# Kernel optimization log

Hardware: AMD Instinct MI355X
Metric: run time of the kernel (lower is better)

## Reference

```python
import jax, jax.numpy as jnp
import numpy as np
import math

L, N, D = 1024, 64, 64
O = 1024

def setup_inputs() -> dict:
    key = jax.random.key(0)
    k1, k2 = jax.random.split(key)
    x = jax.random.normal(k1, (L, N, D), dtype=jnp.float32)
    upfold = jax.random.normal(k2, (O, N, D), dtype=jnp.float32)
    return {"x": x, "upfold": upfold}

def reference(x, upfold):
    # x: [L, N, D], upfold: [O, N, D]
    d = x.shape[-1]
    scale = 1.0 / math.sqrt(d)
    # affinities: [L, O, N]
    affinities = jnp.einsum('lnd,ond->lon', x, upfold) * scale
    # weighted sum with (sigmoid - 0.5) weights: [L, N, D]
    features = jnp.einsum('lon,ond->lnd', jax.nn.sigmoid(affinities) - 0.5, upfold)
    return features
```

## Files before the change

kernel.cpp:

```cpp
#include <hip/hip_runtime.h>
#include <stdint.h>

#define L_DIM 1024
#define N_DIM 64
#define D_DIM 64
#define O_DIM 1024
#define ND    4096
#define NT    8

typedef float    floatx16 __attribute__((ext_vector_type(16)));
typedef _Float16 half8    __attribute__((ext_vector_type(8)));
typedef _Float16 h2       __attribute__((ext_vector_type(2)));
typedef __fp16   fp16x2   __attribute__((ext_vector_type(2)));

#define IMG_BYTES 16384
#define WS_NEEDED ((size_t)N_DIM * 16 * IMG_BYTES)

#define BUF_STRIDE_FB 17920

__device__ __forceinline__ uint32_t pkh2(float a, float b) {
    fp16x2 p = __builtin_amdgcn_cvt_pkrtz(a, b);
    return __builtin_bit_cast(uint32_t, p);
}

__device__ __forceinline__ half8 mk_frag(uint32_t a, uint32_t b, uint32_t c, uint32_t d) {
    union { uint32_t u[4]; half8 v; } U;
    U.u[0] = a; U.u[1] = b; U.u[2] = c; U.u[3] = d;
    return U.v;
}

__device__ __forceinline__ uint32_t psig(float s0, float s1) {
    const h2 HI = {(_Float16)41.6f,        (_Float16)41.6f};
    const h2 LO = {(_Float16)-41.6f,       (_Float16)-41.6f};
    const h2 SC = {(_Float16)0.0625f,      (_Float16)0.0625f};
    const h2 C0 = {(_Float16)0.03099238f,  (_Float16)0.03099238f};
    const h2 C1 = {(_Float16)-0.00842090f, (_Float16)-0.00842090f};
    const h2 C2 = {(_Float16)0.00151845f,  (_Float16)0.00151845f};
    const h2 C3 = {(_Float16)-1.02197e-4f, (_Float16)-1.02197e-4f};
    h2 s = __builtin_bit_cast(h2, pkh2(s0, s1));
    s = __builtin_elementwise_min(s, HI);
    s = __builtin_elementwise_max(s, LO);
    h2 ha = s * SC;
    h2 v  = ha * ha;
    h2 w  = C2 + v * C3;
    w     = C1 + v * w;
    w     = C0 + v * w;
    h2 f  = s * w;
    return __builtin_bit_cast(uint32_t, f);
}

__device__ __forceinline__ void load_tile(const float* ubase, int ot,
                                          int r8, int c, float4* va, float4* vb) {
    const float* pr = ubase + (size_t)(ot * 64 + 2 * r8) * ND + 4 * c;
    #pragma unroll
    for (int j = 0; j < 2; ++j) {
        va[j] = *(const float4*)(pr + (size_t)(32 * j) * ND);
        vb[j] = *(const float4*)(pr + (size_t)(32 * j) * ND + ND);
    }
}

__global__ void __launch_bounds__(256)
conv_kernel(const float* __restrict__ up, unsigned char* __restrict__ img)
{
    const int tid = threadIdx.x;
    const int r8  = tid >> 4;
    const int c   = tid & 15;
    const int n   = blockIdx.x;
    const int ot  = blockIdx.y;

    const float* ubase = up + (size_t)n * D_DIM;
    float4 va[2], vb[2];
    load_tile(ubase, ot, r8, c, va, vb);

    unsigned char* tb = img + (size_t)(n * 16 + ot) * IMG_BYTES;

    const int kk = c >> 2;
    const int hh = (c >> 1) & 1;
    const int co = (c & 1) * 8;
    #pragma unroll
    for (int j = 0; j < 2; ++j) {
        const int o0 = 2 * r8 + 32 * j;
        unsigned char* g1 = tb + j * 4096 + kk * 1024 + co;
        *(uint2*)(g1 + ((o0 & 31) + 32 * hh) * 16) =
            make_uint2(pkh2(va[j].x, va[j].y), pkh2(va[j].z, va[j].w));
        *(uint2*)(g1 + (((o0 + 1) & 31) + 32 * hh) * 16) =
            make_uint2(pkh2(vb[j].x, vb[j].y), pkh2(vb[j].z, vb[j].w));
    }

    #pragma unroll
    for (int j = 0; j < 2; ++j) {
        const int op   = r8 + 16 * j;
        const int g    = op >> 2;
        const int slot = op & 3;
        const int t2   = g >> 2;
        const int c22  = (g >> 1) & 1;
        const int h2i  = g & 1;
        const float* pa = (const float*)&va[j];
        const float* pb = (const float*)&vb[j];
        #pragma unroll
        for (int col = 0; col < 4; ++col) {
            const int d   = 4 * c + col;
            const int r   = d >> 5;
            const int lane = (d & 31) + 32 * h2i;
            *(uint32_t*)(tb + 8192 + t2 * 4096 + c22 * 2048 + r * 1024
                         + lane * 16 + slot * 4) = pkh2(pa[col], pb[col]);
        }
    }
}

__global__ void __launch_bounds__(512, 4)
corr_kernel_c(const float* __restrict__ x, const unsigned char* __restrict__ img,
              float* __restrict__ out)
{
    __shared__ __align__(16) float Xs[128][68];

    const int tid  = threadIdx.x;
    const int lane = tid & 63;
    const int wid  = tid >> 6;
    const int team = wid >> 2;
    const int tw   = wid & 3;
    const int l31  = lane & 31;
    const int h    = lane >> 5;
    const int n    = blockIdx.x;
    const int lb   = blockIdx.y;
    const int lw   = lb * 128 + tw * 32 + l31;

    const unsigned char* gimg = img + (size_t)n * 16 * IMG_BYTES;

    half8 Xf[4];
    {
        const int xr = tid >> 2;
        const int xq = tid & 3;
        const float* xsrc = x + (size_t)(lb * 128 + xr) * ND + n * D_DIM;
        #pragma unroll
        for (int j = 0; j < 4; ++j) {
            const int f4i = xq * 4 + j;
            *(float4*)&Xs[xr][4 * f4i] = *(const float4*)(xsrc + 4 * f4i);
        }
        __syncthreads();
        const int rl = tw * 32 + l31;
        #pragma unroll
        for (int kk = 0; kk < 4; ++kk) {
            float4 f1 = *(const float4*)&Xs[rl][16 * kk + 8 * h];
            float4 f2 = *(const float4*)&Xs[rl][16 * kk + 8 * h + 4];
            Xf[kk] = mk_frag(pkh2(f1.x, f1.y), pkh2(f1.z, f1.w),
                             pkh2(f2.x, f2.y), pkh2(f2.z, f2.w));
        }
        __syncthreads();
    }

    floatx16 F0, F1;
    #pragma unroll
    for (int i = 0; i < 16; ++i) { F0[i] = 0.0f; F1[i] = 0.0f; }

    for (int ot = 0; ot < 16; ++ot) {
        const unsigned char* tb = gimg + (size_t)ot * IMG_BYTES;

        const unsigned char* g1 = tb + team * 4096 + lane * 16;
        half8 Ak[4];
        #pragma unroll
        for (int kk = 0; kk < 4; ++kk)
            Ak[kk] = *(const half8*)(g1 + kk * 1024);

        floatx16 S;
        #pragma unroll
        for (int i2 = 0; i2 < 16; ++i2) S[i2] = 0.0f;
        #pragma unroll
        for (int kk = 0; kk < 4; ++kk)
            S = __builtin_amdgcn_mfma_f32_32x32x16_f16(Ak[kk], Xf[kk], S, 0, 0, 0);

        uint32_t P[8];
        #pragma unroll
        for (int m = 0; m < 8; ++m) P[m] = psig(S[2*m], S[2*m+1]);

        uint32_t R[4];
        #pragma unroll
        for (int c2 = 0; c2 < 2; ++c2) {
            const int t4 = c2 * 4;
            R[2*c2]   = __shfl_xor(h ? P[t4]     : P[t4 + 2], 32);
            R[2*c2+1] = __shfl_xor(h ? P[t4 + 1] : P[t4 + 3], 32);
        }
        const unsigned char* g2 = tb + 8192 + team * 4096 + lane * 16;
        #pragma unroll
        for (int c2 = 0; c2 < 2; ++c2) {
            const int t4 = c2 * 4;
            half8 B = h ? mk_frag(R[2*c2], R[2*c2+1], P[t4 + 2], P[t4 + 3])
                        : mk_frag(P[t4], P[t4 + 1], R[2*c2], R[2*c2+1]);
            half8 A0 = *(const half8*)(g2 + c2 * 2048);
            half8 A1 = *(const half8*)(g2 + c2 * 2048 + 1024);
            F0 = __builtin_amdgcn_mfma_f32_32x32x16_f16(A0, B, F0, 0, 0, 0);
            F1 = __builtin_amdgcn_mfma_f32_32x32x16_f16(A1, B, F1, 0, 0, 0);
        }
    }

    {
        const int row = tw * 32 + l31;
        if (team == 1) {
            #pragma unroll
            for (int q = 0; q < 4; ++q) {
                float4 a; a.x = F0[4*q]; a.y = F0[4*q+1]; a.z = F0[4*q+2]; a.w = F0[4*q+3];
                *(float4*)&Xs[row][8*q + 4*h] = a;
                float4 bq; bq.x = F1[4*q]; bq.y = F1[4*q+1]; bq.z = F1[4*q+2]; bq.w = F1[4*q+3];
                *(float4*)&Xs[row][32 + 8*q + 4*h] = bq;
            }
        }
        __syncthreads();
        if (team == 0) {
            float* op = out + (size_t)lw * ND + n * D_DIM;
            #pragma unroll
            for (int q = 0; q < 4; ++q) {
                float4 t0 = *(const float4*)&Xs[row][8*q + 4*h];
                float4 a; a.x = F0[4*q]   + t0.x; a.y = F0[4*q+1] + t0.y;
                          a.z = F0[4*q+2] + t0.z; a.w = F0[4*q+3] + t0.w;
                *(float4*)(op + 8*q + 4*h) = a;
                float4 t1 = *(const float4*)&Xs[row][32 + 8*q + 4*h];
                float4 bq; bq.x = F1[4*q]   + t1.x; bq.y = F1[4*q+1] + t1.y;
                           bq.z = F1[4*q+2] + t1.z; bq.w = F1[4*q+3] + t1.w;
                *(float4*)(op + 32 + 8*q + 4*h) = bq;
            }
        }
    }
}

__global__ void __launch_bounds__(512, 4)
corr_kernel_fb(const float* __restrict__ x, const float* __restrict__ up,
               float* __restrict__ out)
{
    __shared__ __align__(16) unsigned char smem[4 * BUF_STRIDE_FB];

    const int tid  = threadIdx.x;
    const int lane = tid & 63;
    const int wid  = tid >> 6;
    const int team = wid >> 2;
    const int tw   = wid & 3;
    const int l31  = lane & 31;
    const int h    = lane >> 5;
    const int ttid = tid & 255;
    const int r8   = ttid >> 4;
    const int c    = ttid & 15;
    const int n    = blockIdx.x;
    const int lb   = blockIdx.y;
    const int lw   = lb * 128 + tw * 32 + l31;

    const float* ubase = up + (size_t)n * D_DIM;
    const int ob = team * NT;
    unsigned char* tsmem = smem + team * 2 * BUF_STRIDE_FB;

    float4 va[2], vb[2];
    load_tile(ubase, ob + 0, r8, c, va, vb);

    half8 Xf[4];
    {
        float (*Xs)[68] = (float (*)[68])smem;
        const int xr = tid >> 2;
        const int xq = tid & 3;
        const float* xsrc = x + (size_t)(lb * 128 + xr) * ND + n * D_DIM;
        #pragma unroll
        for (int j = 0; j < 4; ++j) {
            const int f4i = xq * 4 + j;
            *(float4*)&Xs[xr][4 * f4i] = *(const float4*)(xsrc + 4 * f4i);
        }
        __syncthreads();
        const int rl = tw * 32 + l31;
        #pragma unroll
        for (int kk = 0; kk < 4; ++kk) {
            float4 f1 = *(const float4*)&Xs[rl][16 * kk + 8 * h];
            float4 f2 = *(const float4*)&Xs[rl][16 * kk + 8 * h + 4];
            Xf[kk] = mk_frag(pkh2(f1.x, f1.y), pkh2(f1.z, f1.w),
                             pkh2(f2.x, f2.y), pkh2(f2.z, f2.w));
        }
        __syncthreads();
    }

    #pragma unroll
    for (int j = 0; j < 2; ++j) {
        uint16_t (*Ub)[72]  = (uint16_t (*)[72])(tsmem);
        uint32_t (*Ut2)[68] = (uint32_t (*)[68])(tsmem + 9216);
        *(uint2*)&Ub[2*r8 + 32*j][4*c] =
            make_uint2(pkh2(va[j].x, va[j].y), pkh2(va[j].z, va[j].w));
        *(uint2*)&Ub[2*r8 + 32*j + 1][4*c] =
            make_uint2(pkh2(vb[j].x, vb[j].y), pkh2(vb[j].z, vb[j].w));
        *(uint4*)&Ut2[r8 + 16*j][4*c] =
            make_uint4(pkh2(va[j].x, vb[j].x), pkh2(va[j].y, vb[j].y),
                       pkh2(va[j].z, vb[j].z), pkh2(va[j].w, vb[j].w));
    }
    load_tile(ubase, ob + 1, r8, c, va, vb);
    __syncthreads();

    floatx16 F0, F1;
    #pragma unroll
    for (int i = 0; i < 16; ++i) { F0[i] = 0.0f; F1[i] = 0.0f; }

    for (int ot = 0; ot < NT; ++ot) {
        const int b = ot & 1;
        uint16_t (*Ub)[72]   = (uint16_t (*)[72])(tsmem + b * BUF_STRIDE_FB);
        const uint32_t* utp  = (const uint32_t*)(tsmem + b * BUF_STRIDE_FB + 9216);
        uint16_t (*Ubn)[72]  = (uint16_t (*)[72])(tsmem + (b ^ 1) * BUF_STRIDE_FB);
        uint32_t (*Ut2n)[68] = (uint32_t (*)[68])(tsmem + (b ^ 1) * BUF_STRIDE_FB + 9216);

        half8 A0k[4], A1k[4];
        #pragma unroll
        for (int kk = 0; kk < 4; ++kk) {
            A0k[kk] = *(const half8*)&Ub[l31][16 * kk + 8 * h];
            A1k[kk] = *(const half8*)&Ub[32 + l31][16 * kk + 8 * h];
        }

        if (ot + 1 < NT) {
            #pragma unroll
            for (int j = 0; j < 2; ++j) {
                *(uint2*)&Ubn[2*r8 + 32*j][4*c] =
                    make_uint2(pkh2(va[j].x, va[j].y), pkh2(va[j].z, va[j].w));
                *(uint2*)&Ubn[2*r8 + 32*j + 1][4*c] =
                    make_uint2(pkh2(vb[j].x, vb[j].y), pkh2(vb[j].z, vb[j].w));
                *(uint4*)&Ut2n[r8 + 16*j][4*c] =
                    make_uint4(pkh2(va[j].x, vb[j].x), pkh2(va[j].y, vb[j].y),
                               pkh2(va[j].z, vb[j].z), pkh2(va[j].w, vb[j].w));
            }
        }
        if (ot + 2 < NT)
            load_tile(ubase, ob + ot + 2, r8, c, va, vb);

        floatx16 S0, S1;
        #pragma unroll
        for (int i = 0; i < 16; ++i) { S0[i] = 0.0f; S1[i] = 0.0f; }
        #pragma unroll
        for (int kk = 0; kk < 4; ++kk) {
            S0 = __builtin_amdgcn_mfma_f32_32x32x16_f16(A0k[kk], Xf[kk], S0, 0, 0, 0);
            S1 = __builtin_amdgcn_mfma_f32_32x32x16_f16(A1k[kk], Xf[kk], S1, 0, 0, 0);
        }

        uint32_t P[16];
        #pragma unroll
        for (int m = 0; m < 8; ++m) P[m]     = psig(S0[2*m], S0[2*m+1]);
        #pragma unroll
        for (int m = 0; m < 8; ++m) P[8 + m] = psig(S1[2*m], S1[2*m+1]);

        uint32_t R[8];
        #pragma unroll
        for (int c2 = 0; c2 < 4; ++c2) {
            const uint32_t* Q = P + (c2 >> 1) * 8;
            const int t4 = (c2 & 1) * 4;
            R[2*c2]   = __shfl_xor(h ? Q[t4]     : Q[t4 + 2], 32);
            R[2*c2+1] = __shfl_xor(h ? Q[t4 + 1] : Q[t4 + 3], 32);
        }
        #pragma unroll
        for (int c2 = 0; c2 < 4; ++c2) {
            const uint32_t* Q = P + (c2 >> 1) * 8;
            const int t4 = (c2 & 1) * 4;
            half8 B = h ? mk_frag(R[2*c2], R[2*c2+1], Q[t4 + 2], Q[t4 + 3])
                        : mk_frag(Q[t4], Q[t4 + 1], R[2*c2], R[2*c2+1]);
            const int opb = 8 * c2 + 4 * h;
            uint32_t a0[4], a1[4];
            #pragma unroll
            for (int k = 0; k < 4; ++k) {
                a0[k] = utp[(opb + k) * 68 + l31];
                a1[k] = utp[(opb + k) * 68 + 32 + l31];
            }
            half8 A0 = mk_frag(a0[0], a0[1], a0[2], a0[3]);
            half8 A1 = mk_frag(a1[0], a1[1], a1[2], a1[3]);
            F0 = __builtin_amdgcn_mfma_f32_32x32x16_f16(A0, B, F0, 0, 0, 0);
            F1 = __builtin_amdgcn_mfma_f32_32x32x16_f16(A1, B, F1, 0, 0, 0);
        }
        __syncthreads();
    }

    {
        float (*Fs)[68] = (float (*)[68])smem;
        const int row = tw * 32 + l31;
        if (team == 1) {
            #pragma unroll
            for (int q = 0; q < 4; ++q) {
                float4 a; a.x = F0[4*q]; a.y = F0[4*q+1]; a.z = F0[4*q+2]; a.w = F0[4*q+3];
                *(float4*)&Fs[row][8*q + 4*h] = a;
                float4 bq; bq.x = F1[4*q]; bq.y = F1[4*q+1]; bq.z = F1[4*q+2]; bq.w = F1[4*q+3];
                *(float4*)&Fs[row][32 + 8*q + 4*h] = bq;
            }
        }
        __syncthreads();
        if (team == 0) {
            float* op = out + (size_t)lw * ND + n * D_DIM;
            #pragma unroll
            for (int q = 0; q < 4; ++q) {
                float4 t0 = *(const float4*)&Fs[row][8*q + 4*h];
                float4 a; a.x = F0[4*q]   + t0.x; a.y = F0[4*q+1] + t0.y;
                          a.z = F0[4*q+2] + t0.z; a.w = F0[4*q+3] + t0.w;
                *(float4*)(op + 8*q + 4*h) = a;
                float4 t1 = *(const float4*)&Fs[row][32 + 8*q + 4*h];
                float4 bq; bq.x = F1[4*q]   + t1.x; bq.y = F1[4*q+1] + t1.y;
                           bq.z = F1[4*q+2] + t1.z; bq.w = F1[4*q+3] + t1.w;
                *(float4*)(op + 32 + 8*q + 4*h) = bq;
            }
        }
    }
}

extern "C" void kernel_launch(void* const* d_in, const int* in_sizes, int n_in,
                              void* d_out, int out_size, void* d_ws, size_t ws_size,
                              hipStream_t stream)
{
    const float* x  = (const float*)d_in[0];
    const float* up = (const float*)d_in[1];
    float* out      = (float*)d_out;

    if (d_ws != nullptr && ws_size >= WS_NEEDED) {
        unsigned char* img = (unsigned char*)d_ws;
        conv_kernel<<<dim3(N_DIM, 16), dim3(256), 0, stream>>>(up, img);
        corr_kernel_c<<<dim3(N_DIM, L_DIM / 128), dim3(512), 0, stream>>>(x, img, out);
    } else {
        corr_kernel_fb<<<dim3(N_DIM, L_DIM / 128), dim3(512), 0, stream>>>(x, up, out);
    }
}
```

Baseline: 111.6 us.

## Widen corr kernel to 256 rows per block with double-buffered fragment loads

```diff
diff --git a/kernel.cpp b/kernel.cpp
--- a/kernel.cpp
+++ b/kernel.cpp
@@ -99,8 +99,8 @@
         const float* pb = (const float*)&vb[j];
         #pragma unroll
         for (int col = 0; col < 4; ++col) {
-            const int d   = 4 * c + col;
-            const int r   = d >> 5;
+            const int d    = 4 * c + col;
+            const int r    = d >> 5;
             const int lane = (d & 31) + 32 * h2i;
             *(uint32_t*)(tb + 8192 + t2 * 4096 + c22 * 2048 + r * 1024
                          + lane * 16 + slot * 4) = pkh2(pa[col], pb[col]);
@@ -108,11 +108,65 @@
     }
 }
 
-__global__ void __launch_bounds__(512, 4)
-corr_kernel_c(const float* __restrict__ x, const unsigned char* __restrict__ img,
+__device__ __forceinline__ void load_frags(const unsigned char* tb, int team, int lane,
+                                           half8* Ak, half8* G2) {
+    const unsigned char* g1 = tb + team * 4096 + (size_t)lane * 16;
+    #pragma unroll
+    for (int kk = 0; kk < 4; ++kk)
+        Ak[kk] = *(const half8*)(g1 + kk * 1024);
+    const unsigned char* g2 = tb + 8192 + team * 4096 + (size_t)lane * 16;
+    #pragma unroll
+    for (int i = 0; i < 4; ++i)
+        G2[i] = *(const half8*)(g2 + i * 1024);
+}
+
+__device__ __forceinline__ void compute_tile(const half8* Ak, const half8* G2,
+                                             const half8* Xf0, const half8* Xf1, int h,
+                                             floatx16& F00, floatx16& F01,
+                                             floatx16& F10, floatx16& F11)
+{
+    floatx16 S0, S1;
+    #pragma unroll
+    for (int i = 0; i < 16; ++i) { S0[i] = 0.0f; S1[i] = 0.0f; }
+    #pragma unroll
+    for (int kk = 0; kk < 4; ++kk) {
+        S0 = __builtin_amdgcn_mfma_f32_32x32x16_f16(Ak[kk], Xf0[kk], S0, 0, 0, 0);
+        S1 = __builtin_amdgcn_mfma_f32_32x32x16_f16(Ak[kk], Xf1[kk], S1, 0, 0, 0);
+    }
+
+    uint32_t P0[8], P1[8];
+    #pragma unroll
+    for (int m = 0; m < 8; ++m) { P0[m] = psig(S0[2*m], S0[2*m+1]);
+                                  P1[m] = psig(S1[2*m], S1[2*m+1]); }
+
+    uint32_t R0[4], R1[4];
+    #pragma unroll
+    for (int c2 = 0; c2 < 2; ++c2) {
+        const int t4 = c2 * 4;
+        R0[2*c2]   = __shfl_xor(h ? P0[t4]     : P0[t4 + 2], 32);
+        R0[2*c2+1] = __shfl_xor(h ? P0[t4 + 1] : P0[t4 + 3], 32);
+        R1[2*c2]   = __shfl_xor(h ? P1[t4]     : P1[t4 + 2], 32);
+        R1[2*c2+1] = __shfl_xor(h ? P1[t4 + 1] : P1[t4 + 3], 32);
+    }
+    #pragma unroll
+    for (int c2 = 0; c2 < 2; ++c2) {
+        const int t4 = c2 * 4;
+        half8 B0 = h ? mk_frag(R0[2*c2], R0[2*c2+1], P0[t4 + 2], P0[t4 + 3])
+                     : mk_frag(P0[t4], P0[t4 + 1], R0[2*c2], R0[2*c2+1]);
+        half8 B1 = h ? mk_frag(R1[2*c2], R1[2*c2+1], P1[t4 + 2], P1[t4 + 3])
+                     : mk_frag(P1[t4], P1[t4 + 1], R1[2*c2], R1[2*c2+1]);
+        F00 = __builtin_amdgcn_mfma_f32_32x32x16_f16(G2[2*c2],     B0, F00, 0, 0, 0);
+        F01 = __builtin_amdgcn_mfma_f32_32x32x16_f16(G2[2*c2 + 1], B0, F01, 0, 0, 0);
+        F10 = __builtin_amdgcn_mfma_f32_32x32x16_f16(G2[2*c2],     B1, F10, 0, 0, 0);
+        F11 = __builtin_amdgcn_mfma_f32_32x32x16_f16(G2[2*c2 + 1], B1, F11, 0, 0, 0);
+    }
+}
+
+__global__ void __launch_bounds__(512, 2)
+corr_kernel_w(const float* __restrict__ x, const unsigned char* __restrict__ img,
               float* __restrict__ out)
 {
-    __shared__ __align__(16) float Xs[128][68];
+    __shared__ __align__(16) float Xs[256][68];
 
     const int tid  = threadIdx.x;
     const int lane = tid & 63;
@@ -123,100 +177,86 @@
     const int h    = lane >> 5;
     const int n    = blockIdx.x;
     const int lb   = blockIdx.y;
-    const int lw   = lb * 128 + tw * 32 + l31;
 
     const unsigned char* gimg = img + (size_t)n * 16 * IMG_BYTES;
 
-    half8 Xf[4];
+    half8 Xf0[4], Xf1[4];
     {
-        const int xr = tid >> 2;
-        const int xq = tid & 3;
-        const float* xsrc = x + (size_t)(lb * 128 + xr) * ND + n * D_DIM;
-        #pragma unroll
-        for (int j = 0; j < 4; ++j) {
-            const int f4i = xq * 4 + j;
+        const int xr = tid >> 1;
+        const int xh = tid & 1;
+        const float* xsrc = x + (size_t)(lb * 256 + xr) * ND + n * D_DIM;
+        #pragma unroll
+        for (int j = 0; j < 8; ++j) {
+            const int f4i = xh * 8 + j;
             *(float4*)&Xs[xr][4 * f4i] = *(const float4*)(xsrc + 4 * f4i);
         }
         __syncthreads();
-        const int rl = tw * 32 + l31;
+        const int rl0 = tw * 64 + l31;
+        const int rl1 = rl0 + 32;
         #pragma unroll
         for (int kk = 0; kk < 4; ++kk) {
-            float4 f1 = *(const float4*)&Xs[rl][16 * kk + 8 * h];
-            float4 f2 = *(const float4*)&Xs[rl][16 * kk + 8 * h + 4];
-            Xf[kk] = mk_frag(pkh2(f1.x, f1.y), pkh2(f1.z, f1.w),
-                             pkh2(f2.x, f2.y), pkh2(f2.z, f2.w));
-        }
-        __syncthreads();
-    }
-
-    floatx16 F0, F1;
-    #pragma unroll
-    for (int i = 0; i < 16; ++i) { F0[i] = 0.0f; F1[i] = 0.0f; }
-
-    for (int ot = 0; ot < 16; ++ot) {
-        const unsigned char* tb = gimg + (size_t)ot * IMG_BYTES;
-
-        const unsigned char* g1 = tb + team * 4096 + lane * 16;
-        half8 Ak[4];
-        #pragma unroll
-        for (int kk = 0; kk < 4; ++kk)
-            Ak[kk] = *(const half8*)(g1 + kk * 1024);
-
-        floatx16 S;
-        #pragma unroll
-        for (int i2 = 0; i2 < 16; ++i2) S[i2] = 0.0f;
-        #pragma unroll
-        for (int kk = 0; kk < 4; ++kk)
-            S = __builtin_amdgcn_mfma_f32_32x32x16_f16(Ak[kk], Xf[kk], S, 0, 0, 0);
-
-        uint32_t P[8];
-        #pragma unroll
-        for (int m = 0; m < 8; ++m) P[m] = psig(S[2*m], S[2*m+1]);
-
-        uint32_t R[4];
-        #pragma unroll
-        for (int c2 = 0; c2 < 2; ++c2) {
-            const int t4 = c2 * 4;
-            R[2*c2]   = __shfl_xor(h ? P[t4]     : P[t4 + 2], 32);
-            R[2*c2+1] = __shfl_xor(h ? P[t4 + 1] : P[t4 + 3], 32);
-        }
-        const unsigned char* g2 = tb + 8192 + team * 4096 + lane * 16;
-        #pragma unroll
-        for (int c2 = 0; c2 < 2; ++c2) {
-            const int t4 = c2 * 4;
-            half8 B = h ? mk_frag(R[2*c2], R[2*c2+1], P[t4 + 2], P[t4 + 3])
-                        : mk_frag(P[t4], P[t4 + 1], R[2*c2], R[2*c2+1]);
-            half8 A0 = *(const half8*)(g2 + c2 * 2048);
-            half8 A1 = *(const half8*)(g2 + c2 * 2048 + 1024);
-            F0 = __builtin_amdgcn_mfma_f32_32x32x16_f16(A0, B, F0, 0, 0, 0);
-            F1 = __builtin_amdgcn_mfma_f32_32x32x16_f16(A1, B, F1, 0, 0, 0);
-        }
+            float4 f1 = *(const float4*)&Xs[rl0][16 * kk + 8 * h];
+            float4 f2 = *(const float4*)&Xs[rl0][16 * kk + 8 * h + 4];
+            Xf0[kk] = mk_frag(pkh2(f1.x, f1.y), pkh2(f1.z, f1.w),
+                              pkh2(f2.x, f2.y), pkh2(f2.z, f2.w));
+            float4 f3 = *(const float4*)&Xs[rl1][16 * kk + 8 * h];
+            float4 f4v = *(const float4*)&Xs[rl1][16 * kk + 8 * h + 4];
+            Xf1[kk] = mk_frag(pkh2(f3.x, f3.y), pkh2(f3.z, f3.w),
+                              pkh2(f4v.x, f4v.y), pkh2(f4v.z, f4v.w));
+        }
+        __syncthreads();
+    }
+
+    floatx16 F00, F01, F10, F11;
+    #pragma unroll
+    for (int i = 0; i < 16; ++i) { F00[i] = 0.0f; F01[i] = 0.0f;
+                                   F10[i] = 0.0f; F11[i] = 0.0f; }
+
+    half8 AkE[4], G2E[4], AkO[4], G2O[4];
+    load_frags(gimg, team, lane, AkE, G2E);
+    for (int ot = 0; ot < 16; ot += 2) {
+        load_frags(gimg + (size_t)(ot + 1) * IMG_BYTES, team, lane, AkO, G2O);
+        compute_tile(AkE, G2E, Xf0, Xf1, h, F00, F01, F10, F11);
+        if (ot + 2 < 16)
+            load_frags(gimg + (size_t)(ot + 2) * IMG_BYTES, team, lane, AkE, G2E);
+        compute_tile(AkO, G2O, Xf0, Xf1, h, F00, F01, F10, F11);
     }
 
     {
-        const int row = tw * 32 + l31;
         if (team == 1) {
             #pragma unroll
-            for (int q = 0; q < 4; ++q) {
-                float4 a; a.x = F0[4*q]; a.y = F0[4*q+1]; a.z = F0[4*q+2]; a.w = F0[4*q+3];
-                *(float4*)&Xs[row][8*q + 4*h] = a;
-                float4 bq; bq.x = F1[4*q]; bq.y = F1[4*q+1]; bq.z = F1[4*q+2]; bq.w = F1[4*q+3];
-                *(float4*)&Xs[row][32 + 8*q + 4*h] = bq;
+            for (int lh = 0; lh < 2; ++lh) {
+                const int row = tw * 64 + lh * 32 + l31;
+                const floatx16& A = lh ? F10 : F00;
+                const floatx16& Bq = lh ? F11 : F01;
+                #pragma unroll
+                for (int q = 0; q < 4; ++q) {
+                    float4 a; a.x = A[4*q]; a.y = A[4*q+1]; a.z = A[4*q+2]; a.w = A[4*q+3];
+                    *(float4*)&Xs[row][8*q + 4*h] = a;
+                    float4 b2; b2.x = Bq[4*q]; b2.y = Bq[4*q+1]; b2.z = Bq[4*q+2]; b2.w = Bq[4*q+3];
+                    *(float4*)&Xs[row][32 + 8*q + 4*h] = b2;
+                }
             }
         }
         __syncthreads();
         if (team == 0) {
-            float* op = out + (size_t)lw * ND + n * D_DIM;
-            #pragma unroll
-            for (int q = 0; q < 4; ++q) {
-                float4 t0 = *(const float4*)&Xs[row][8*q + 4*h];
-                float4 a; a.x = F0[4*q]   + t0.x; a.y = F0[4*q+1] + t0.y;
-                          a.z = F0[4*q+2] + t0.z; a.w = F0[4*q+3] + t0.w;
-                *(float4*)(op + 8*q + 4*h) = a;
-                float4 t1 = *(const float4*)&Xs[row][32 + 8*q + 4*h];
-                float4 bq; bq.x = F1[4*q]   + t1.x; bq.y = F1[4*q+1] + t1.y;
-                           bq.z = F1[4*q+2] + t1.z; bq.w = F1[4*q+3] + t1.w;
-                *(float4*)(op + 32 + 8*q + 4*h) = bq;
+            #pragma unroll
+            for (int lh = 0; lh < 2; ++lh) {
+                const int row = tw * 64 + lh * 32 + l31;
+                const floatx16& A = lh ? F10 : F00;
+                const floatx16& Bq = lh ? F11 : F01;
+                float* op = out + (size_t)(lb * 256 + row) * ND + n * D_DIM;
+                #pragma unroll
+                for (int q = 0; q < 4; ++q) {
+                    float4 t0 = *(const float4*)&Xs[row][8*q + 4*h];
+                    float4 a; a.x = A[4*q]   + t0.x; a.y = A[4*q+1] + t0.y;
+                              a.z = A[4*q+2] + t0.z; a.w = A[4*q+3] + t0.w;
+                    *(float4*)(op + 8*q + 4*h) = a;
+                    float4 t1 = *(const float4*)&Xs[row][32 + 8*q + 4*h];
+                    float4 b2; b2.x = Bq[4*q]   + t1.x; b2.y = Bq[4*q+1] + t1.y;
+                               b2.z = Bq[4*q+2] + t1.z; b2.w = Bq[4*q+3] + t1.w;
+                    *(float4*)(op + 32 + 8*q + 4*h) = b2;
+                }
             }
         }
     }
@@ -405,7 +445,7 @@
     if (d_ws != nullptr && ws_size >= WS_NEEDED) {
         unsigned char* img = (unsigned char*)d_ws;
         conv_kernel<<<dim3(N_DIM, 16), dim3(256), 0, stream>>>(up, img);
-        corr_kernel_c<<<dim3(N_DIM, L_DIM / 128), dim3(512), 0, stream>>>(x, img, out);
+        corr_kernel_w<<<dim3(N_DIM, L_DIM / 256), dim3(512), 0, stream>>>(x, img, out);
     } else {
         corr_kernel_fb<<<dim3(N_DIM, L_DIM / 128), dim3(512), 0, stream>>>(x, up, out);
     }
```

Measured after the change: 108.9 us. 2.5% less time.
